# Kernel optimization log

Hardware: AMD Instinct MI355X
Metric: run time of the kernel (lower is better)

The kernel has to match this reference:

```python
import jax, jax.numpy as jnp
import numpy as np

ALPHA, GAMMA, EPS = 0.25, 2.0, 1e-8
COST_CLASS, COST_BBOX, COST_GIOU = 2.0, 5.0, 2.0


def box_cxcywh_to_xyxy(b):
    cx, cy, w, h = jnp.split(b, 4, axis=-1)
    return jnp.concatenate([cx - 0.5 * w, cy - 0.5 * h, cx + 0.5 * w, cy + 0.5 * h], axis=-1)


def setup_inputs() -> dict:
    key = jax.random.key(0)
    k1, k2, k3, k4 = jax.random.split(key, 4)
    bs, Q, C, T = 16, 900, 80, 1600
    return {
        "pred_logits": jax.random.normal(k1, (bs, Q, C), jnp.float32),
        "pred_boxes": jax.random.uniform(k2, (bs, Q, 4), jnp.float32),
        "tgt_labels": jax.random.randint(k3, (T,), 0, C),
        "tgt_boxes": jax.random.uniform(k4, (T, 4), jnp.float32),
        "g_size": 3,
    }


def reference(pred_logits, pred_boxes, tgt_labels, tgt_boxes, g_size):
    bs, Q, _ = pred_logits.shape
    # focal classification cost (use_focal=True path)
    p = jax.nn.sigmoid(pred_logits.reshape(bs * Q, -1))  # [N, C]
    neg = (1.0 - ALPHA) * p ** GAMMA * (-jnp.log(1.0 - p + EPS))
    pos = ALPHA * (1.0 - p) ** GAMMA * (-jnp.log(p + EPS))
    cost_class = (pos - neg)[:, tgt_labels]  # [N, T]
    # L1 box cost (cdist p=1)
    out_bbox = pred_boxes.reshape(bs * Q, 4)
    cost_bbox = jnp.abs(out_bbox[:, None, :] - tgt_bbox_b(tgt_boxes)).sum(-1)  # [N, T]
    # GIoU cost
    b1 = box_cxcywh_to_xyxy(out_bbox)  # [N, 4]
    b2 = box_cxcywh_to_xyxy(tgt_boxes)  # [T, 4]
    area1 = (b1[:, 2] - b1[:, 0]) * (b1[:, 3] - b1[:, 1])
    area2 = (b2[:, 2] - b2[:, 0]) * (b2[:, 3] - b2[:, 1])
    lt = jnp.maximum(b1[:, None, :2], b2[None, :, :2])
    rb = jnp.minimum(b1[:, None, 2:], b2[None, :, 2:])
    wh = jnp.clip(rb - lt, 0.0)
    inter = wh[..., 0] * wh[..., 1]
    union = area1[:, None] + area2[None, :] - inter
    iou = inter / union
    elt = jnp.minimum(b1[:, None, :2], b2[None, :, :2])
    erb = jnp.maximum(b1[:, None, 2:], b2[None, :, 2:])
    ewh = jnp.clip(erb - elt, 0.0)
    earea = ewh[..., 0] * ewh[..., 1]
    giou = iou - (earea - union) / earea
    # weighted total cost, then group reduction (note: original names it Cmin but takes max over the group dim)
    Cmat = COST_BBOX * cost_bbox + COST_CLASS * cost_class + COST_GIOU * (-giou)
    Cmin = Cmat.reshape(bs, Q // g_size, g_size, -1).max(axis=2)  # [bs, Q//g, T]
    return Cmin


def tgt_bbox_b(tgt_boxes):
    return tgt_boxes[None, :, :]
```

## Files before the change

kernel.cpp:

```cpp
#include <hip/hip_runtime.h>

#define ALPHA 0.25f
#define EPS   1e-8f

constexpr int BS = 16;
constexpr int QN = 900;
constexpr int CN = 80;
constexpr int GS = 3;
constexpr int QG_PER_BLOCK = 4;
constexpr int ROWS = QG_PER_BLOCK * GS;
constexpr int NT_THREADS = 256;

__global__ __launch_bounds__(NT_THREADS) void fused_cost_kernel(
    const float* __restrict__ pred_logits,
    const float* __restrict__ pred_boxes,
    const int*   __restrict__ tgt_labels,
    const float* __restrict__ tgt_boxes,
    float*       __restrict__ out,
    int T)
{
    __shared__ float4 s_raw[ROWS];
    __shared__ float4 s_xy [ROWS];
    __shared__ float  s_cc [ROWS * CN];

    const int tid = threadIdx.x;
    const int qg0 = blockIdx.x * QG_PER_BLOCK;
    const int b   = blockIdx.y;
    const int n0  = b * QN + qg0 * GS;

    if (tid < ROWS) {
        const float4 r = ((const float4*)pred_boxes)[n0 + tid];
        s_raw[tid] = r;
        s_xy[tid]  = make_float4(r.x - 0.5f * r.z, r.y - 0.5f * r.w,
                                 r.x + 0.5f * r.z, r.y + 0.5f * r.w);
    }
    const float* lg0 = pred_logits + (size_t)n0 * CN;
    #pragma unroll
    for (int k = tid; k < ROWS * CN; k += NT_THREADS) {
        float x = lg0[k];
        float p = __fdividef(1.0f, 1.0f + __expf(-x));
        float omp = 1.0f - p;
        float pos = ALPHA * omp * omp * (-__logf(p + EPS));
        float neg = (1.0f - ALPHA) * p * p * (-__logf(omp + EPS));
        s_cc[k] = pos - neg;
    }
    __syncthreads();

    const int qgTotal = QN / GS;
    const size_t outBase = (size_t)(b * qgTotal + qg0) * T;

    for (int t = tid; t < T; t += NT_THREADS) {
        const float4 tr = ((const float4*)tgt_boxes)[t];
        const float tx0 = tr.x - 0.5f * tr.z, ty0 = tr.y - 0.5f * tr.w;
        const float tx1 = tr.x + 0.5f * tr.z, ty1 = tr.y + 0.5f * tr.w;
        const float ta  = tr.z * tr.w;
        const int lab   = tgt_labels[t];

        #pragma unroll
        for (int j = 0; j < QG_PER_BLOCK; ++j) {
            float m = -3.402823466e+38f;
            #pragma unroll
            for (int g = 0; g < GS; ++g) {
                const int idx = j * GS + g;
                const float4 pr = s_raw[idx];
                const float4 px = s_xy[idx];
                const float  ccv = s_cc[idx * CN + lab];
                const float  pa = pr.z * pr.w;

                float l1 = fabsf(pr.x - tr.x) + fabsf(pr.y - tr.y)
                         + fabsf(pr.z - tr.z) + fabsf(pr.w - tr.w);

                float iw = fminf(px.z, tx1) - fmaxf(px.x, tx0);
                float ih = fminf(px.w, ty1) - fmaxf(px.y, ty0);
                float inter = fmaxf(iw, 0.0f) * fmaxf(ih, 0.0f);
                float uni   = pa + ta - inter;

                float ew = fmaxf(px.z, tx1) - fminf(px.x, tx0);
                float eh = fmaxf(px.w, ty1) - fminf(px.y, ty0);
                float earea = ew * eh;

                float giou = __fdividef(inter, uni) + __fdividef(uni, earea) - 1.0f;

                float cost = 5.0f * l1 + 2.0f * ccv - 2.0f * giou;
                m = fmaxf(m, cost);
            }
            out[outBase + (size_t)j * T + t] = m;
        }
    }
}

extern "C" void kernel_launch(void* const* d_in, const int* in_sizes, int n_in,
                              void* d_out, int out_size, void* d_ws, size_t ws_size,
                              hipStream_t stream) {
    const float* pred_logits = (const float*)d_in[0];
    const float* pred_boxes  = (const float*)d_in[1];
    const int*   tgt_labels  = (const int*)d_in[2];
    const float* tgt_boxes   = (const float*)d_in[3];

    const int T = in_sizes[2];
    float* out = (float*)d_out;

    dim3 grid((QN / GS) / QG_PER_BLOCK, BS);
    fused_cost_kernel<<<grid, NT_THREADS, 0, stream>>>(
        pred_logits, pred_boxes, tgt_labels, tgt_boxes, out, T);
}
```

Measured before the change: 107.7 us.

## Split targets across blocks, keep pred boxes in registers, transpose class cost

```diff
diff --git a/kernel.cpp b/kernel.cpp
--- a/kernel.cpp
+++ b/kernel.cpp
@@ -10,6 +10,7 @@
 constexpr int QG_PER_BLOCK = 4;
 constexpr int ROWS = QG_PER_BLOCK * GS;
 constexpr int NT_THREADS = 256;
+constexpr int TSPLIT = 2;
 
 __global__ __launch_bounds__(NT_THREADS) void fused_cost_kernel(
     const float* __restrict__ pred_logits,
@@ -19,42 +20,53 @@
     float*       __restrict__ out,
     int T)
 {
-    __shared__ float4 s_raw[ROWS];
-    __shared__ float4 s_xy [ROWS];
-    __shared__ float  s_cc [ROWS * CN];
+    __shared__ __align__(16) float s_cc_t[CN * ROWS];
 
     const int tid = threadIdx.x;
-    const int qg0 = blockIdx.x * QG_PER_BLOCK;
-    const int b   = blockIdx.y;
+    const int qg0 = blockIdx.y * QG_PER_BLOCK;
+    const int b   = blockIdx.z;
     const int n0  = b * QN + qg0 * GS;
 
-    if (tid < ROWS) {
-        const float4 r = ((const float4*)pred_boxes)[n0 + tid];
-        s_raw[tid] = r;
-        s_xy[tid]  = make_float4(r.x - 0.5f * r.z, r.y - 0.5f * r.w,
-                                 r.x + 0.5f * r.z, r.y + 0.5f * r.w);
-    }
     const float* lg0 = pred_logits + (size_t)n0 * CN;
-    #pragma unroll
     for (int k = tid; k < ROWS * CN; k += NT_THREADS) {
+        const int r = k / CN, c = k - r * CN;
         float x = lg0[k];
         float p = __fdividef(1.0f, 1.0f + __expf(-x));
         float omp = 1.0f - p;
         float pos = ALPHA * omp * omp * (-__logf(p + EPS));
         float neg = (1.0f - ALPHA) * p * p * (-__logf(omp + EPS));
-        s_cc[k] = pos - neg;
+        s_cc_t[c * ROWS + r] = pos - neg;
+    }
+
+    float Pcx[ROWS], Pcy[ROWS], Pw[ROWS], Ph[ROWS];
+    float Px0[ROWS], Py0[ROWS], Px1[ROWS], Py1[ROWS];
+    #pragma unroll
+    for (int r = 0; r < ROWS; ++r) {
+        const float4 pb = ((const float4*)pred_boxes)[n0 + r];
+        Pcx[r] = pb.x;  Pcy[r] = pb.y;  Pw[r] = pb.z;  Ph[r] = pb.w;
+        Px0[r] = pb.x - 0.5f * pb.z;  Py0[r] = pb.y - 0.5f * pb.w;
+        Px1[r] = pb.x + 0.5f * pb.z;  Py1[r] = pb.y + 0.5f * pb.w;
     }
     __syncthreads();
 
+    const int tChunk = T / TSPLIT;
+    const int t0 = blockIdx.x * tChunk;
+    const int tEnd = t0 + tChunk;
     const int qgTotal = QN / GS;
     const size_t outBase = (size_t)(b * qgTotal + qg0) * T;
 
-    for (int t = tid; t < T; t += NT_THREADS) {
+    for (int t = t0 + tid; t < tEnd; t += NT_THREADS) {
         const float4 tr = ((const float4*)tgt_boxes)[t];
+        const int lab   = tgt_labels[t];
         const float tx0 = tr.x - 0.5f * tr.z, ty0 = tr.y - 0.5f * tr.w;
         const float tx1 = tr.x + 0.5f * tr.z, ty1 = tr.y + 0.5f * tr.w;
         const float ta  = tr.z * tr.w;
-        const int lab   = tgt_labels[t];
+
+        const float4* ccp = (const float4*)&s_cc_t[lab * ROWS];
+        const float4 c0 = ccp[0], c1 = ccp[1], c2 = ccp[2];
+        const float ccv[ROWS] = { c0.x, c0.y, c0.z, c0.w,
+                                  c1.x, c1.y, c1.z, c1.w,
+                                  c2.x, c2.y, c2.z, c2.w };
 
         #pragma unroll
         for (int j = 0; j < QG_PER_BLOCK; ++j) {
@@ -62,26 +74,24 @@
             #pragma unroll
             for (int g = 0; g < GS; ++g) {
                 const int idx = j * GS + g;
-                const float4 pr = s_raw[idx];
-                const float4 px = s_xy[idx];
-                const float  ccv = s_cc[idx * CN + lab];
-                const float  pa = pr.z * pr.w;
 
-                float l1 = fabsf(pr.x - tr.x) + fabsf(pr.y - tr.y)
-                         + fabsf(pr.z - tr.z) + fabsf(pr.w - tr.w);
+                float l1 = fabsf(Pcx[idx] - tr.x) + fabsf(Pcy[idx] - tr.y)
+                         + fabsf(Pw[idx]  - tr.z) + fabsf(Ph[idx]  - tr.w);
 
-                float iw = fminf(px.z, tx1) - fmaxf(px.x, tx0);
-                float ih = fminf(px.w, ty1) - fmaxf(px.y, ty0);
+                float iw = fminf(Px1[idx], tx1) - fmaxf(Px0[idx], tx0);
+                float ih = fminf(Py1[idx], ty1) - fmaxf(Py0[idx], ty0);
                 float inter = fmaxf(iw, 0.0f) * fmaxf(ih, 0.0f);
-                float uni   = pa + ta - inter;
+                float uni   = Pw[idx] * Ph[idx] + ta - inter;
 
-                float ew = fmaxf(px.z, tx1) - fminf(px.x, tx0);
-                float eh = fmaxf(px.w, ty1) - fminf(px.y, ty0);
+                float ew = fmaxf(Px1[idx], tx1) - fminf(Px0[idx], tx0);
+                float eh = fmaxf(Py1[idx], ty1) - fminf(Py0[idx], ty0);
                 float earea = ew * eh;
 
-                float giou = __fdividef(inter, uni) + __fdividef(uni, earea) - 1.0f;
+                float num = fmaf(inter, earea, uni * uni);
+                float den = uni * earea;
+                float g2  = 2.0f * __fdividef(num, den);
 
-                float cost = 5.0f * l1 + 2.0f * ccv - 2.0f * giou;
+                float cost = fmaf(5.0f, l1, fmaf(2.0f, ccv[idx], 2.0f - g2));
                 m = fmaxf(m, cost);
             }
             out[outBase + (size_t)j * T + t] = m;
@@ -100,7 +110,7 @@
     const int T = in_sizes[2];
     float* out = (float*)d_out;
 
-    dim3 grid((QN / GS) / QG_PER_BLOCK, BS);
+    dim3 grid(TSPLIT, (QN / GS) / QG_PER_BLOCK, BS);
     fused_cost_kernel<<<grid, NT_THREADS, 0, stream>>>(
         pred_logits, pred_boxes, tgt_labels, tgt_boxes, out, T);
 }
```

Result: faster. 102.4 us (-4.9%).
